# Performance work log

Hardware: AMD Instinct MI355X
Metric: run time of the kernel (lower is better)

## Reference

```python
import jax, jax.numpy as jnp
import numpy as np

B, C, H, W = 16, 512, 24, 24


def setup_inputs() -> dict:
    key = jax.random.key(0)
    ks = jax.random.split(key, 7)
    s = 0.02
    return {
        "x5": jax.random.normal(ks[0], (B, C, H, W), jnp.float32),
        "conv_w": jax.random.normal(ks[1], (C, C), jnp.float32) * s,
        "conv_b": jax.random.normal(ks[2], (C,), jnp.float32) * s,
        "q_w": jax.random.normal(ks[3], (C, C), jnp.float32) * s,
        "q_b": jax.random.normal(ks[4], (C,), jnp.float32) * s,
        "k_w": jax.random.normal(ks[5], (C, C), jnp.float32) * s,
        "k_b": jax.random.normal(ks[6], (C,), jnp.float32) * s,
    }


def _conv1x1(x, w, b):
    # 1x1 conv == channel matmul: (O,C) x (B,C,H,W) -> (B,O,H,W)
    return jnp.einsum('oc,bchw->bohw', w, x) + b[None, :, None, None]


def reference(x5, conv_w, conv_b, q_w, q_b, k_w, k_b):
    Bb, Cc, Hh, Ww = x5.shape
    scale = 1.0 / (Cc ** 0.5)
    x5 = _conv1x1(x5, conv_w, conv_b) + x5
    # my_SS2D source was not provided in the module; treated as identity (see notes)
    x00 = x5
    # cross-batch correlation: queries (B*H*W, C), keys (B, C, H*W)
    q = _conv1x1(x00, q_w, q_b).reshape(Bb, Cc, Hh * Ww).transpose(0, 2, 1).reshape(Bb * Hh * Ww, Cc)
    k = _conv1x1(x00, k_w, k_b).reshape(Bb, Cc, Hh * Ww)
    # scores: (B*H*W, B, H*W); max over locations, mean over images
    scores = jnp.einsum('nc,bcm->nbm', q, k) * scale
    x_w = scores.max(axis=-1).mean(axis=-1).reshape(Bb, Hh * Ww)
    x_w = jax.nn.softmax(x_w, axis=-1)
    # channel-wise L2 normalize (F.normalize, eps=1e-12)
    nrm = jnp.sqrt(jnp.sum(x5 * x5, axis=1, keepdims=True))
    norm0 = x5 / jnp.maximum(nrm, 1e-12)
    # top-1 (equality-based) seed mask per image
    x_w_max = x_w.max(axis=-1, keepdims=True)
    mask = (x_w == x_w_max).astype(x5.dtype).reshape(Bb, 1, Hh, Ww)
    seeds = (norm0 * mask).sum(axis=(2, 3))  # (B, C)
    # seeded 1x1-conv correlation (eval mode -> relu): (B, B_seeds, H, W)
    corr = jax.nn.relu(jnp.einsum('bchw,sc->bshw', norm0, seeds)).mean(axis=1).reshape(Bb, Hh * Ww)
    mn = corr.min(axis=-1, keepdims=True)
    mx = corr.max(axis=-1, keepdims=True)
    cormap = ((corr - mn) / (mx - mn + 1e-12)).reshape(Bb, 1, Hh, Ww)
    x51 = x5 * cormap
    proto1 = jnp.mean(x51, axis=(0, 2, 3), keepdims=True)  # (1, C, 1, 1)
    return (x5, proto1, x5 * proto1 + x51, mask)
```

## Files before the change

### kernel.cpp

```cpp
#include <hip/hip_runtime.h>
#include <math.h>

#define BB   16
#define CC   512
#define HWW  576
#define NN   9216
#define CHW  (CC*HWW)
#define TOT  (BB*CHW)
#define SCALE 0.044194173824159216f
#define FRAGB 9437184

typedef __attribute__((ext_vector_type(8))) __bf16 bf16x8;
typedef __attribute__((ext_vector_type(4))) float f32x4;

#define AS1 __attribute__((address_space(1)))
#define AS3 __attribute__((address_space(3)))

static __device__ __forceinline__ void gload_lds16(const void* g, void* l)
{
    __builtin_amdgcn_global_load_lds((AS1 const void*)g, (AS3 void*)l, 16, 0, 0);
}


__global__ __launch_bounds__(256)
void prep_x_kernel(const float* __restrict__ X, __bf16* __restrict__ Xhi,
                   __bf16* __restrict__ Xlo)
{
    int g = blockIdx.x * 256 + threadIdx.x;
    int n = g % NN;
    int co = g / NN;
    int c0 = co * 8;
    int bimg = n / HWW, mm = n % HWW;
    const float* src = X + (size_t)bimg * CHW + mm;
    union { __bf16 h[8]; float4 f4; } uh, ul;
#pragma unroll
    for (int j = 0; j < 8; j++) {
        float v = src[(size_t)(c0 + j) * HWW];
        __bf16 h = (__bf16)v;
        uh.h[j] = h;
        ul.h[j] = (__bf16)(v - (float)h);
    }
    int Cb = c0 >> 6, s = (c0 >> 5) & 1, q8 = (c0 >> 3) & 3;
    int T = n >> 6, g4 = (n >> 4) & 3, Lm = n & 15;
    size_t off = (size_t)(Cb * 144 + T) * 4096 + (s * 4 + g4) * 512 + (size_t)((q8 << 4) | Lm) * 8;
    *(float4*)&Xhi[off] = uh.f4;
    *(float4*)&Xlo[off] = ul.f4;
}

__global__ __launch_bounds__(256)
void prep_w_kernel(const float* __restrict__ cw, const float* __restrict__ qw,
                   const float* __restrict__ kw, __bf16* __restrict__ cwhi,
                   __bf16* __restrict__ cwlo, __bf16* __restrict__ qwf,
                   __bf16* __restrict__ kwf)
{
    int y = blockIdx.y;
    const float* W = (y == 0) ? cw : (y == 1) ? qw : kw;
    __bf16* dh = (y == 0) ? cwhi : (y == 1) ? qwf : kwf;
    int g = blockIdx.x * 256 + threadIdx.x;
    int o = g >> 6;
    int c0 = (g & 63) * 8;
    union { __bf16 h[8]; float4 f4; } uh, ul;
#pragma unroll
    for (int j = 0; j < 8; j++) {
        float v = W[(size_t)o * CC + c0 + j];
        __bf16 h = (__bf16)v;
        uh.h[j] = h;
        ul.h[j] = (__bf16)(v - (float)h);
    }
    int Cb = c0 >> 6, s = (c0 >> 5) & 1, q8 = (c0 >> 3) & 3;
    int To = o >> 6, g4 = (o >> 4) & 3, Lm = o & 15;
    size_t off = (size_t)(Cb * 8 + To) * 4096 + (s * 4 + g4) * 512 + (size_t)((q8 << 4) | Lm) * 8;
    *(float4*)&dh[off] = uh.f4;
    if (y == 0) *(float4*)&cwlo[off] = ul.f4;
}

__global__ __launch_bounds__(256)
void conv1_mfma_kernel(const float* __restrict__ X, const __bf16* __restrict__ Whi,
                       const __bf16* __restrict__ Wlo, const __bf16* __restrict__ Xhi,
                       const __bf16* __restrict__ Xlo, const float* __restrict__ bias,
                       float* __restrict__ Y, __bf16* __restrict__ Yfrag)
{
    __shared__ __bf16 lAh[8192], lAl[8192], lBh[8192], lBl[8192];
    int tid = threadIdx.x, lane = tid & 63, wv = tid >> 6;
    int wo = wv >> 1, wm = wv & 1;
    int m0 = blockIdx.x * 128;
    int o0 = blockIdx.y * 128;
    int oT0 = blockIdx.y * 2, mT0 = blockIdx.x * 2;

    f32x4 acc[4][4];
#pragma unroll
    for (int i = 0; i < 4; i++)
#pragma unroll
        for (int j = 0; j < 4; j++) acc[i][j] = (f32x4){0.f, 0.f, 0.f, 0.f};

    for (int Cb = 0; Cb < 8; Cb++) {
        const float4* gAh = (const float4*)(Whi + (size_t)(Cb * 8 + oT0) * 4096);
        const float4* gAl = (const float4*)(Wlo + (size_t)(Cb * 8 + oT0) * 4096);
        const float4* gBh = (const float4*)(Xhi + (size_t)(Cb * 144 + mT0) * 4096);
        const float4* gBl = (const float4*)(Xlo + (size_t)(Cb * 144 + mT0) * 4096);
#pragma unroll
        for (int i = 0; i < 4; i++) {
            int eb = wv * 256 + i * 64;
            gload_lds16(gAh + eb + lane, (float4*)lAh + eb);
            gload_lds16(gAl + eb + lane, (float4*)lAl + eb);
            gload_lds16(gBh + eb + lane, (float4*)lBh + eb);
            gload_lds16(gBl + eb + lane, (float4*)lBl + eb);
        }
        __syncthreads();
#pragma unroll
        for (int s = 0; s < 2; s++) {
            bf16x8 ah[4], al[4], bh[4], bl[4];
#pragma unroll
            for (int ga = 0; ga < 4; ga++) {
                ah[ga] = *(const bf16x8*)&lAh[wo * 4096 + (s * 4 + ga) * 512 + lane * 8];
                al[ga] = *(const bf16x8*)&lAl[wo * 4096 + (s * 4 + ga) * 512 + lane * 8];
            }
#pragma unroll
            for (int gb = 0; gb < 4; gb++) {
                bh[gb] = *(const bf16x8*)&lBh[wm * 4096 + (s * 4 + gb) * 512 + lane * 8];
                bl[gb] = *(const bf16x8*)&lBl[wm * 4096 + (s * 4 + gb) * 512 + lane * 8];
            }
#pragma unroll
            for (int ga = 0; ga < 4; ga++)
#pragma unroll
                for (int gb = 0; gb < 4; gb++) {
                    acc[ga][gb] = __builtin_amdgcn_mfma_f32_16x16x32_bf16(ah[ga], bh[gb], acc[ga][gb], 0, 0, 0);
                    acc[ga][gb] = __builtin_amdgcn_mfma_f32_16x16x32_bf16(ah[ga], bl[gb], acc[ga][gb], 0, 0, 0);
                    acc[ga][gb] = __builtin_amdgcn_mfma_f32_16x16x32_bf16(al[ga], bh[gb], acc[ga][gb], 0, 0, 0);
                }
        }
        __syncthreads();
    }

    int quad = lane >> 4, col = lane & 15;
#pragma unroll
    for (int ga = 0; ga < 4; ga++) {
        int ob = o0 + wo * 64 + ga * 16 + quad * 4;
        float bs[4];
#pragma unroll
        for (int r = 0; r < 4; r++) bs[r] = bias[ob + r];
        int Cb2 = ob >> 6, s2 = (ob >> 5) & 1, q8 = (ob >> 3) & 3, j0 = ob & 7;
#pragma unroll
        for (int gb = 0; gb < 4; gb++) {
            int n = m0 + wm * 64 + gb * 16 + col;
            int T = n >> 6, g4 = (n >> 4) & 3, Lm = n & 15;
            int bimg = n / HWW, mm = n % HWW;
            size_t xb = (size_t)bimg * CHW + mm;
            union { __bf16 h[4]; float2 f2; } u;
#pragma unroll
            for (int r = 0; r < 4; r++) {
                float v = acc[ga][gb][r] + bs[r] + X[xb + (size_t)(ob + r) * HWW];
                Y[xb + (size_t)(ob + r) * HWW] = v;
                u.h[r] = (__bf16)v;
            }
            *(float2*)&Yfrag[(size_t)(Cb2 * 144 + T) * 4096 + (s2 * 4 + g4) * 512 + (size_t)((q8 << 4) | Lm) * 8 + j0] = u.f2;
        }
    }
}

__global__ __launch_bounds__(256)
void convqk_mfma_kernel(const __bf16* __restrict__ qwf, const __bf16* __restrict__ kwf,
                        const float* __restrict__ qb, const float* __restrict__ kb,
                        const __bf16* __restrict__ Xf, __bf16* __restrict__ Oq,
                        __bf16* __restrict__ Ok)
{
    const __bf16* Wf = blockIdx.z ? kwf : qwf;
    const float* bias = blockIdx.z ? kb : qb;
    __bf16* Of = blockIdx.z ? Ok : Oq;

    __shared__ __bf16 lA[8192], lB[8192];
    int tid = threadIdx.x, lane = tid & 63, wv = tid >> 6;
    int wo = wv >> 1, wm = wv & 1;
    int m0 = blockIdx.x * 128;
    int o0 = blockIdx.y * 128;
    int oT0 = blockIdx.y * 2, mT0 = blockIdx.x * 2;

    f32x4 acc[4][4];
#pragma unroll
    for (int i = 0; i < 4; i++)
#pragma unroll
        for (int j = 0; j < 4; j++) acc[i][j] = (f32x4){0.f, 0.f, 0.f, 0.f};

    for (int Cb = 0; Cb < 8; Cb++) {
        const float4* gA = (const float4*)(Wf + (size_t)(Cb * 8 + oT0) * 4096);
        const float4* gB = (const float4*)(Xf + (size_t)(Cb * 144 + mT0) * 4096);
#pragma unroll
        for (int i = 0; i < 4; i++) {
            int eb = wv * 256 + i * 64;
            gload_lds16(gA + eb + lane, (float4*)lA + eb);
            gload_lds16(gB + eb + lane, (float4*)lB + eb);
        }
        __syncthreads();
#pragma unroll
        for (int s = 0; s < 2; s++) {
            bf16x8 af[4], bf[4];
#pragma unroll
            for (int ga = 0; ga < 4; ga++)
                af[ga] = *(const bf16x8*)&lA[wo * 4096 + (s * 4 + ga) * 512 + lane * 8];
#pragma unroll
            for (int gb = 0; gb < 4; gb++)
                bf[gb] = *(const bf16x8*)&lB[wm * 4096 + (s * 4 + gb) * 512 + lane * 8];
#pragma unroll
            for (int ga = 0; ga < 4; ga++)
#pragma unroll
                for (int gb = 0; gb < 4; gb++)
                    acc[ga][gb] = __builtin_amdgcn_mfma_f32_16x16x32_bf16(af[ga], bf[gb], acc[ga][gb], 0, 0, 0);
        }
        __syncthreads();
    }

    int quad = lane >> 4, col = lane & 15;
#pragma unroll
    for (int ga = 0; ga < 4; ga++) {
        int ob = o0 + wo * 64 + ga * 16 + quad * 4;
        float bs[4];
#pragma unroll
        for (int r = 0; r < 4; r++) bs[r] = bias[ob + r];
        int Cb2 = ob >> 6, s2 = (ob >> 5) & 1, q8 = (ob >> 3) & 3, j0 = ob & 7;
#pragma unroll
        for (int gb = 0; gb < 4; gb++) {
            int n = m0 + wm * 64 + gb * 16 + col;
            int T = n >> 6, g4 = (n >> 4) & 3, Lm = n & 15;
            union { __bf16 h[4]; float2 f2; } u;
#pragma unroll
            for (int r = 0; r < 4; r++) u.h[r] = (__bf16)(acc[ga][gb][r] + bs[r]);
            *(float2*)&Of[(size_t)(Cb2 * 144 + T) * 4096 + (s2 * 4 + g4) * 512 + (size_t)((q8 << 4) | Lm) * 8 + j0] = u.f2;
        }
    }
}

__global__ __launch_bounds__(256)
void scores_mfma_kernel(const __bf16* __restrict__ Qf, const __bf16* __restrict__ Kf,
                        float* __restrict__ maxv3, int bidoff)
{
    __shared__ __bf16 ldsQ[8192];
    __shared__ __bf16 ldsK[12288];

    int tid = threadIdx.x, lane = tid & 63, wv = tid >> 6;
    int wq = wv >> 1, wk = wv & 1;
    int bid = blockIdx.x + bidoff;
    int by = bid % 48;
    int bx = bid / 48;
    int n0 = bx * 128;
    int b = by / 3, mt = by % 3;

    f32x4 acc[4][6];
#pragma unroll
    for (int ga = 0; ga < 4; ga++)
#pragma unroll
        for (int t = 0; t < 6; t++) acc[ga][t] = (f32x4){0.f, 0.f, 0.f, 0.f};

    const float4* gq = (const float4*)(Qf + (size_t)(bx * 2) * 4096);
    const float4* gk = (const float4*)(Kf + (size_t)(b * 9 + mt * 3) * 4096);
    const int CSTRIDE = 144 * 4096 / 8;

    for (int C = 0; C < 8; C++) {
#pragma unroll
        for (int i = 0; i < 4; i++) {
            int eb = wv * 256 + i * 64;
            gload_lds16(gq + eb + lane, (float4*)ldsQ + eb);
        }
#pragma unroll
        for (int i = 0; i < 6; i++) {
            int eb = wv * 384 + i * 64;
            gload_lds16(gk + eb + lane, (float4*)ldsK + eb);
        }
        gq += CSTRIDE;
        gk += CSTRIDE;
        __syncthreads();
#pragma unroll
        for (int s = 0; s < 2; s++) {
            bf16x8 af[4];
#pragma unroll
            for (int ga = 0; ga < 4; ga++)
                af[ga] = *(const bf16x8*)&ldsQ[wq * 4096 + (s * 4 + ga) * 512 + lane * 8];
#pragma unroll
            for (int t = 0; t < 6; t++) {
                int mkl = wk * 96 + t * 16;
                bf16x8 bfr = *(const bf16x8*)&ldsK[(mkl >> 6) * 4096 + (s * 4 + ((mkl >> 4) & 3)) * 512 + lane * 8];
#pragma unroll
                for (int ga = 0; ga < 4; ga++)
                    acc[ga][t] = __builtin_amdgcn_mfma_f32_16x16x32_bf16(af[ga], bfr, acc[ga][t], 0, 0, 0);
            }
        }
        __syncthreads();
    }

    float mg[4][4];
#pragma unroll
    for (int ga = 0; ga < 4; ga++)
#pragma unroll
        for (int r = 0; r < 4; r++) {
            float v = acc[ga][0][r];
#pragma unroll
            for (int t = 1; t < 6; t++) v = fmaxf(v, acc[ga][t][r]);
            mg[ga][r] = v;
        }
#pragma unroll
    for (int off = 1; off < 16; off <<= 1)
#pragma unroll
        for (int ga = 0; ga < 4; ga++)
#pragma unroll
            for (int r = 0; r < 4; r++)
                mg[ga][r] = fmaxf(mg[ga][r], __shfl_xor(mg[ga][r], off, 64));

    float (*redbuf)[2] = (float (*)[2])ldsQ;
    if ((lane & 15) == 0) {
        int quad = lane >> 4;
#pragma unroll
        for (int ga = 0; ga < 4; ga++)
#pragma unroll
            for (int r = 0; r < 4; r++)
                redbuf[wq * 64 + ga * 16 + quad * 4 + r][wk] = mg[ga][r];
    }
    __syncthreads();
    if (tid < 128) {
        float rv = fmaxf(redbuf[tid][0], redbuf[tid][1]) * SCALE;
        maxv3[((size_t)(n0 + tid) * BB + b) * 3 + mt] = rv;
    }
}

__global__ __launch_bounds__(576)
void topk_kernel(const float* __restrict__ maxv3, int* __restrict__ cand)
{
    __shared__ float sv[576];
    __shared__ float rv_[64];
    __shared__ int ri_[64];
    int bi = blockIdx.x, m = threadIdx.x;
    int n = bi * HWW + m;
    float v = 0.f;
#pragma unroll
    for (int t = 0; t < BB; t++) {
        const float* p = maxv3 + ((size_t)n * BB + t) * 3;
        v += fmaxf(fmaxf(p[0], p[1]), p[2]);
    }
    sv[m] = v;
    __syncthreads();
    for (int r = 0; r < 4; r++) {
        if (m < 64) {
            float bv = sv[m]; int bidx = m;
            for (int j = m + 64; j < 576; j += 64)
                if (sv[j] > bv) { bv = sv[j]; bidx = j; }
            rv_[m] = bv; ri_[m] = bidx;
        }
        __syncthreads();
        if (m == 0) {
            float bv = rv_[0]; int bidx = ri_[0];
            for (int j = 1; j < 64; j++)
                if (rv_[j] > bv) { bv = rv_[j]; bidx = ri_[j]; }
            cand[bi * 4 + r] = bidx;
            sv[bidx] = -3.4e38f;
        }
        __syncthreads();
    }
}

__global__ __launch_bounds__(256)
void refine_q_kernel(const float* __restrict__ x5, const float* __restrict__ qw,
                     const float* __restrict__ qb, const int* __restrict__ cand,
                     float* __restrict__ q_all)
{
    int og = blockIdx.x, cd = blockIdx.y;
    int bi = cd >> 2;
    int mstar = cand[cd];
    int tid = threadIdx.x, w = tid >> 6, lane = tid & 63;
    __shared__ float xcol[512];
    __shared__ float qrows[64];
    xcol[tid]       = x5[(size_t)bi * CHW + tid * HWW + mstar];
    xcol[tid + 256] = x5[(size_t)bi * CHW + (tid + 256) * HWW + mstar];
    __syncthreads();
#pragma unroll
    for (int i = 0; i < 16; i++) {
        int r = og * 64 + w * 16 + i;
        float p = 0.f;
#pragma unroll
        for (int it = 0; it < 8; it++) {
            int c = lane + it * 64;
            p = fmaf(qw[(size_t)r * 512 + c], xcol[c], p);
        }
        for (int off = 32; off; off >>= 1) p += __shfl_down(p, off, 64);
        if (lane == 0) qrows[w * 16 + i] = p;
    }
    __syncthreads();
    if (tid < 64) q_all[(size_t)cd * 512 + og * 64 + tid] = qrows[tid] + qb[og * 64 + tid];
}

__global__ __launch_bounds__(256)
void refine_u2_kernel(const float* __restrict__ kw, const float* __restrict__ kb,
                      const float* __restrict__ q_all, float* __restrict__ u_all,
                      float* __restrict__ qkbg)
{
    int tg = blockIdx.x, cd = blockIdx.y;
    int tid = threadIdx.x;
    __shared__ float qs[512];
    qs[tid]       = q_all[(size_t)cd * 512 + tid];
    qs[tid + 256] = q_all[(size_t)cd * 512 + tid + 256];
    __syncthreads();
    int t = tg * 256 + tid;
    float u = 0.f;
    for (int o = 0; o < 512; o++)
        u = fmaf(kw[(size_t)o * 512 + t], qs[o], u);
    u_all[(size_t)cd * 512 + t] = u;
    if (tg == 0) {
        float pk = qs[tid] * kb[tid] + qs[tid + 256] * kb[tid + 256];
        for (int off = 32; off; off >>= 1) pk += __shfl_down(pk, off, 64);
        __shared__ float pr[4];
        if ((tid & 63) == 0) pr[tid >> 6] = pk;
        __syncthreads();
        if (tid == 0) qkbg[cd] = pr[0] + pr[1] + pr[2] + pr[3];
    }
}

__global__ __launch_bounds__(256)
void refine_max_kernel(const float* __restrict__ x5, const float* __restrict__ u_all,
                       float* __restrict__ maxex9)
{
    int bp = blockIdx.x, cg = blockIdx.y, mc = blockIdx.z;
    int tid = threadIdx.x, mi = tid & 63, cs = tid >> 6;
    int m0 = mc * 64;
    __shared__ float us[16 * 512];
    __shared__ float red[256];
    for (int e = tid; e < 16 * 512; e += 256) us[e] = u_all[(size_t)cg * 16 * 512 + e];
    __syncthreads();

    float acc[16];
#pragma unroll
    for (int j = 0; j < 16; j++) acc[j] = 0.f;
    const float* xb = x5 + (size_t)bp * CHW + m0 + mi;
    for (int cc = 0; cc < 128; cc++) {
        int c = cs * 128 + cc;
        float x = xb[(size_t)c * HWW];
#pragma unroll
        for (int j = 0; j < 16; j++)
            acc[j] = fmaf(us[j * 512 + c], x, acc[j]);
    }

#pragma unroll
    for (int j = 0; j < 16; j++) {
        red[tid] = acc[j];
        __syncthreads();
        if (tid < 64) {
            float v = red[tid] + red[tid + 64] + red[tid + 128] + red[tid + 192];
            for (int off = 32; off; off >>= 1) v = fmaxf(v, __shfl_xor(v, off, 64));
            if (tid == 0) maxex9[((size_t)(cg * 16 + j) * BB + bp) * 9 + mc] = v;
        }
        __syncthreads();
    }
}

__global__ __launch_bounds__(576)
void mask_kernel(const float* __restrict__ maxex9, const float* __restrict__ qkbg,
                 const int* __restrict__ cand, float* __restrict__ maskout)
{
    int bi = blockIdx.x, m = threadIdx.x;
    __shared__ float ve[4];
    __shared__ int chosen;
    if (m < 4) {
        int cd = bi * 4 + m;
        float sacc = 0.f;
#pragma unroll
        for (int t = 0; t < BB; t++) {
            const float* p = maxex9 + ((size_t)cd * BB + t) * 9;
            float mv = p[0];
#pragma unroll
            for (int z = 1; z < 9; z++) mv = fmaxf(mv, p[z]);
            sacc += mv;
        }
        ve[m] = sacc * (1.f / 16.f) + qkbg[cd];
    }
    __syncthreads();
    if (m == 0) {
        int best = 0; float bv = ve[0];
        for (int j = 1; j < 4; j++) if (ve[j] > bv) { bv = ve[j]; best = j; }
        chosen = cand[bi * 4 + best];
    }
    __syncthreads();
    maskout[bi * HWW + m] = (m == chosen) ? 1.f : 0.f;
}

__global__ __launch_bounds__(256)
void norm_kernel(const float* __restrict__ X5, float* __restrict__ invb)
{
    int b = blockIdx.y;
    int m0 = blockIdx.x * 64;
    int mi = threadIdx.x & 63, cs = threadIdx.x >> 6;
    float s = 0.f;
    for (int c = cs; c < CC; c += 4) {
        float x = X5[b * CHW + c * HWW + m0 + mi];
        s = fmaf(x, x, s);
    }
    __shared__ float red[4][64];
    red[cs][mi] = s;
    __syncthreads();
    if (cs == 0) {
        float t = red[0][mi] + red[1][mi] + red[2][mi] + red[3][mi];
        invb[b * HWW + m0 + mi] = 1.0f / fmaxf(sqrtf(t), 1e-12f);
    }
}

__global__ __launch_bounds__(256)
void seeds_kernel(const float* __restrict__ X5, const float* __restrict__ invb,
                  const float* __restrict__ maskf, float* __restrict__ seeds)
{
    int s = blockIdx.y;
    int c = blockIdx.x * 4 + (threadIdx.x >> 6);
    int mi = threadIdx.x & 63;
    float acc = 0.f;
    for (int mt = 0; mt < 9; mt++) {
        int m = mt * 64 + mi;
        float w = invb[s * HWW + m] * maskf[s * HWW + m];
        acc = fmaf(X5[s * CHW + c * HWW + m], w, acc);
    }
    for (int off = 32; off > 0; off >>= 1) acc += __shfl_down(acc, off, 64);
    if (mi == 0) seeds[s * CC + c] = acc;
}

__global__ __launch_bounds__(256)
void corr_kernel(const float* __restrict__ X5, const float* __restrict__ invb,
                 const float* __restrict__ seeds, float* __restrict__ corr)
{
    __shared__ float sd[16 * 512];
    __shared__ float xs[64][65];
    __shared__ float red[4][64];
    int b = blockIdx.y;
    int m0 = blockIdx.x * 64;
    int tid = threadIdx.x;
    int mi = tid & 63, sg = tid >> 6;

    for (int e = tid; e < 16 * 512; e += 256) sd[e] = seeds[e];

    float acc[4] = {0.f, 0.f, 0.f, 0.f};
    for (int c0 = 0; c0 < CC; c0 += 64) {
        __syncthreads();
        for (int e = tid; e < 4096; e += 256) {
            int mm = e & 63, kk = e >> 6;
            xs[kk][mm] = X5[b * CHW + (c0 + kk) * HWW + m0 + mm];
        }
        __syncthreads();
#pragma unroll
        for (int kk = 0; kk < 64; kk++) {
            float xv = xs[kk][mi];
#pragma unroll
            for (int t = 0; t < 4; t++)
                acc[t] = fmaf(xv, sd[(sg * 4 + t) * CC + c0 + kk], acc[t]);
        }
    }
    float r = 0.f;
#pragma unroll
    for (int t = 0; t < 4; t++) r += fmaxf(acc[t], 0.f);
    red[sg][mi] = r;
    __syncthreads();
    if (sg == 0) {
        float tot = red[0][mi] + red[1][mi] + red[2][mi] + red[3][mi];
        corr[b * HWW + m0 + mi] = invb[b * HWW + m0 + mi] * tot * (1.0f / 16.0f);
    }
}

__global__ __launch_bounds__(576)
void cormap_kernel(const float* __restrict__ corr, float* __restrict__ cormap)
{
    __shared__ float sv[576];
    __shared__ float smn[64], smx[64];
    __shared__ float s_mn, s_mx;
    int b = blockIdx.x;
    int m = threadIdx.x;
    float v = corr[b * HWW + m];
    sv[m] = v;
    __syncthreads();
    if (m < 64) {
        float mn = sv[m], mx = sv[m];
        for (int j = m + 64; j < 576; j += 64) { mn = fminf(mn, sv[j]); mx = fmaxf(mx, sv[j]); }
        smn[m] = mn; smx[m] = mx;
    }
    __syncthreads();
    if (m == 0) {
        float mn = smn[0], mx = smx[0];
        for (int j = 1; j < 64; j++) { mn = fminf(mn, smn[j]); mx = fmaxf(mx, smx[j]); }
        s_mn = mn; s_mx = mx;
    }
    __syncthreads();
    cormap[b * HWW + m] = (v - s_mn) / (s_mx - s_mn + 1e-12f);
}

__global__ __launch_bounds__(256)
void proto_kernel(const float* __restrict__ X5, const float* __restrict__ cormap,
                  float* __restrict__ proto1)
{
    int c = blockIdx.x;
    int tid = threadIdx.x;
    float acc = 0.f;
    for (int p = tid; p < NN; p += 256) {
        int b = p / HWW, m = p % HWW;
        acc = fmaf(X5[b * CHW + c * HWW + m], cormap[p], acc);
    }
    for (int off = 32; off > 0; off >>= 1) acc += __shfl_down(acc, off, 64);
    __shared__ float red[4];
    if ((tid & 63) == 0) red[tid >> 6] = acc;
    __syncthreads();
    if (tid == 0) proto1[c] = (red[0] + red[1] + red[2] + red[3]) * (1.0f / (float)NN);
}

__global__ __launch_bounds__(256)
void final_kernel(const float* __restrict__ X5, const float* __restrict__ proto1,
                  const float* __restrict__ cormap, float* __restrict__ out3)
{
    int idx = blockIdx.x * 256 + threadIdx.x;
    if (idx >= TOT) return;
    int b = idx / CHW;
    int r = idx % CHW;
    int c = r / HWW;
    int m = r % HWW;
    float x = X5[idx];
    out3[idx] = x * (proto1[c] + cormap[b * HWW + m]);
}

extern "C" void kernel_launch(void* const* d_in, const int* in_sizes, int n_in,
                              void* d_out, int out_size, void* d_ws, size_t ws_size,
                              hipStream_t stream)
{
    const float* x  = (const float*)d_in[0];
    const float* cw = (const float*)d_in[1];
    const float* cb = (const float*)d_in[2];
    const float* qw = (const float*)d_in[3];
    const float* qb = (const float*)d_in[4];
    const float* kw = (const float*)d_in[5];
    const float* kb = (const float*)d_in[6];

    float* out     = (float*)d_out;
    float* x5o     = out;
    float* proto1  = out + TOT;
    float* out3    = out + TOT + 512;
    float* maskout = out + TOT + 512 + TOT;

    char* o3 = (char*)out3;
    __bf16* xlo    = (__bf16*)o3;
    __bf16* qfrag  = (__bf16*)o3;
    __bf16* x5frag = (__bf16*)(o3 + FRAGB);

    char* ws = (char*)d_ws;
    __bf16* xhi   = (__bf16*)ws;
    __bf16* kfrag = (__bf16*)ws;
    __bf16* cwhi  = (__bf16*)(ws + FRAGB);
    __bf16* cwlo  = (__bf16*)(ws + FRAGB + 524288);
    __bf16* qwf   = (__bf16*)(ws + FRAGB + 2 * 524288);
    __bf16* kwf   = (__bf16*)(ws + FRAGB + 3 * 524288);
    char* p = ws + FRAGB + 4 * 524288;
    float* maxv3  = (float*)p;   p += (size_t)NN * BB * 3 * 4;
    int*   cand   = (int*)p;     p += 256;
    float* q_all  = (float*)p;   p += 64 * 512 * 4;
    float* u_all  = (float*)p;   p += 64 * 512 * 4;
    float* qkbg   = (float*)p;   p += 256;
    float* maxex9 = (float*)p;   p += 64 * BB * 9 * 4;
    float* invb   = (float*)p;   p += NN * 4;
    float* corr   = (float*)p;   p += NN * 4;
    float* cmap   = (float*)p;   p += NN * 4;
    float* seeds  = (float*)p;   p += BB * CC * 4;

    prep_x_kernel<<<NN * 64 / 256, 256, 0, stream>>>(x, xhi, xlo);
    prep_w_kernel<<<dim3(128, 3), 256, 0, stream>>>(cw, qw, kw, cwhi, cwlo, qwf, kwf);

    conv1_mfma_kernel<<<dim3(NN / 128, 4), 256, 0, stream>>>(x, cwhi, cwlo, xhi, xlo, cb, x5o, x5frag);
    convqk_mfma_kernel<<<dim3(NN / 128, 4, 2), 256, 0, stream>>>(qwf, kwf, qb, kb, x5frag, qfrag, kfrag);

    scores_mfma_kernel<<<1728, 256, 0, stream>>>(qfrag, kfrag, maxv3, 0);
    scores_mfma_kernel<<<1728, 256, 0, stream>>>(qfrag, kfrag, maxv3, 1728);

    topk_kernel<<<BB, HWW, 0, stream>>>(maxv3, cand);
    refine_q_kernel<<<dim3(8, 64), 256, 0, stream>>>(x5o, qw, qb, cand, q_all);
    refine_u2_kernel<<<dim3(2, 64), 256, 0, stream>>>(kw, kb, q_all, u_all, qkbg);
    refine_max_kernel<<<dim3(BB, 4, 9), 256, 0, stream>>>(x5o, u_all, maxex9);
    mask_kernel<<<BB, HWW, 0, stream>>>(maxex9, qkbg, cand, maskout);

    norm_kernel<<<dim3(9, BB), 256, 0, stream>>>(x5o, invb);
    seeds_kernel<<<dim3(CC / 4, BB), 256, 0, stream>>>(x5o, invb, maskout, seeds);
    corr_kernel<<<dim3(9, BB), 256, 0, stream>>>(x5o, invb, seeds, corr);
    cormap_kernel<<<BB, HWW, 0, stream>>>(corr, cmap);
    proto_kernel<<<CC, 256, 0, stream>>>(x5o, cmap, proto1);
    final_kernel<<<(TOT + 255) / 256, 256, 0, stream>>>(x5o, proto1, cmap, out3);
}
```

Baseline: 387.9 us.

## Load conv weights directly, merge refine kernels, direct seed gather, restructure reductions

The two conv MFMA kernels now read weight fragments straight from global memory into registers instead of staging them through LDS, which cuts LDS use and copy traffic. The two scores launches become one, and the q and u refine kernels are fused into a single per-candidate kernel. Seeds are gathered directly at the chosen index instead of a masked reduction over all positions. The refine_max reduction now uses a single barrier, proto drops its per-element div/mod, and final_kernel uses a 2D grid without index division. Direct global weight loads inside the MFMA loop could add latency if caching does not hide it.

```diff
diff --git a/kernel.cpp b/kernel.cpp
--- a/kernel.cpp
+++ b/kernel.cpp
@@ -80,7 +80,7 @@
                        const __bf16* __restrict__ Xlo, const float* __restrict__ bias,
                        float* __restrict__ Y, __bf16* __restrict__ Yfrag)
 {
-    __shared__ __bf16 lAh[8192], lAl[8192], lBh[8192], lBl[8192];
+    __shared__ __bf16 lBh[8192], lBl[8192];
     int tid = threadIdx.x, lane = tid & 63, wv = tid >> 6;
     int wo = wv >> 1, wm = wv & 1;
     int m0 = blockIdx.x * 128;
@@ -94,26 +94,24 @@
         for (int j = 0; j < 4; j++) acc[i][j] = (f32x4){0.f, 0.f, 0.f, 0.f};
 
     for (int Cb = 0; Cb < 8; Cb++) {
-        const float4* gAh = (const float4*)(Whi + (size_t)(Cb * 8 + oT0) * 4096);
-        const float4* gAl = (const float4*)(Wlo + (size_t)(Cb * 8 + oT0) * 4096);
         const float4* gBh = (const float4*)(Xhi + (size_t)(Cb * 144 + mT0) * 4096);
         const float4* gBl = (const float4*)(Xlo + (size_t)(Cb * 144 + mT0) * 4096);
 #pragma unroll
         for (int i = 0; i < 4; i++) {
             int eb = wv * 256 + i * 64;
-            gload_lds16(gAh + eb + lane, (float4*)lAh + eb);
-            gload_lds16(gAl + eb + lane, (float4*)lAl + eb);
             gload_lds16(gBh + eb + lane, (float4*)lBh + eb);
             gload_lds16(gBl + eb + lane, (float4*)lBl + eb);
         }
+        const __bf16* Ah = Whi + (size_t)(Cb * 8 + oT0 + wo) * 4096 + lane * 8;
+        const __bf16* Al = Wlo + (size_t)(Cb * 8 + oT0 + wo) * 4096 + lane * 8;
         __syncthreads();
 #pragma unroll
         for (int s = 0; s < 2; s++) {
             bf16x8 ah[4], al[4], bh[4], bl[4];
 #pragma unroll
             for (int ga = 0; ga < 4; ga++) {
-                ah[ga] = *(const bf16x8*)&lAh[wo * 4096 + (s * 4 + ga) * 512 + lane * 8];
-                al[ga] = *(const bf16x8*)&lAl[wo * 4096 + (s * 4 + ga) * 512 + lane * 8];
+                ah[ga] = *(const bf16x8*)&Ah[(s * 4 + ga) * 512];
+                al[ga] = *(const bf16x8*)&Al[(s * 4 + ga) * 512];
             }
 #pragma unroll
             for (int gb = 0; gb < 4; gb++) {
@@ -168,7 +166,7 @@
     const float* bias = blockIdx.z ? kb : qb;
     __bf16* Of = blockIdx.z ? Ok : Oq;
 
-    __shared__ __bf16 lA[8192], lB[8192];
+    __shared__ __bf16 lB[8192];
     int tid = threadIdx.x, lane = tid & 63, wv = tid >> 6;
     int wo = wv >> 1, wm = wv & 1;
     int m0 = blockIdx.x * 128;
@@ -182,21 +180,20 @@
         for (int j = 0; j < 4; j++) acc[i][j] = (f32x4){0.f, 0.f, 0.f, 0.f};
 
     for (int Cb = 0; Cb < 8; Cb++) {
-        const float4* gA = (const float4*)(Wf + (size_t)(Cb * 8 + oT0) * 4096);
         const float4* gB = (const float4*)(Xf + (size_t)(Cb * 144 + mT0) * 4096);
 #pragma unroll
         for (int i = 0; i < 4; i++) {
             int eb = wv * 256 + i * 64;
-            gload_lds16(gA + eb + lane, (float4*)lA + eb);
             gload_lds16(gB + eb + lane, (float4*)lB + eb);
         }
+        const __bf16* Aw = Wf + (size_t)(Cb * 8 + oT0 + wo) * 4096 + lane * 8;
         __syncthreads();
 #pragma unroll
         for (int s = 0; s < 2; s++) {
             bf16x8 af[4], bf[4];
 #pragma unroll
             for (int ga = 0; ga < 4; ga++)
-                af[ga] = *(const bf16x8*)&lA[wo * 4096 + (s * 4 + ga) * 512 + lane * 8];
+                af[ga] = *(const bf16x8*)&Aw[(s * 4 + ga) * 512];
 #pragma unroll
             for (int gb = 0; gb < 4; gb++)
                 bf[gb] = *(const bf16x8*)&lB[wm * 4096 + (s * 4 + gb) * 512 + lane * 8];
@@ -231,14 +228,14 @@
 
 __global__ __launch_bounds__(256)
 void scores_mfma_kernel(const __bf16* __restrict__ Qf, const __bf16* __restrict__ Kf,
-                        float* __restrict__ maxv3, int bidoff)
+                        float* __restrict__ maxv3)
 {
     __shared__ __bf16 ldsQ[8192];
     __shared__ __bf16 ldsK[12288];
 
     int tid = threadIdx.x, lane = tid & 63, wv = tid >> 6;
     int wq = wv >> 1, wk = wv & 1;
-    int bid = blockIdx.x + bidoff;
+    int bid = blockIdx.x;
     int by = bid % 48;
     int bx = bid / 48;
     int n0 = bx * 128;
@@ -356,22 +353,21 @@
 }
 
 __global__ __launch_bounds__(256)
-void refine_q_kernel(const float* __restrict__ x5, const float* __restrict__ qw,
-                     const float* __restrict__ qb, const int* __restrict__ cand,
-                     float* __restrict__ q_all)
-{
-    int og = blockIdx.x, cd = blockIdx.y;
+void refine_qu_kernel(const float* __restrict__ x5, const float* __restrict__ qw,
+                      const float* __restrict__ qb, const float* __restrict__ kw,
+                      const float* __restrict__ kb, const int* __restrict__ cand,
+                      float* __restrict__ u_all, float* __restrict__ qkbg)
+{
+    int cd = blockIdx.x;
     int bi = cd >> 2;
     int mstar = cand[cd];
     int tid = threadIdx.x, w = tid >> 6, lane = tid & 63;
-    __shared__ float xcol[512];
-    __shared__ float qrows[64];
+    __shared__ float xcol[512], qv[512];
     xcol[tid]       = x5[(size_t)bi * CHW + tid * HWW + mstar];
     xcol[tid + 256] = x5[(size_t)bi * CHW + (tid + 256) * HWW + mstar];
     __syncthreads();
-#pragma unroll
-    for (int i = 0; i < 16; i++) {
-        int r = og * 64 + w * 16 + i;
+    for (int i = 0; i < 128; i++) {
+        int r = w * 128 + i;
         float p = 0.f;
 #pragma unroll
         for (int it = 0; it < 8; it++) {
@@ -379,36 +375,23 @@
             p = fmaf(qw[(size_t)r * 512 + c], xcol[c], p);
         }
         for (int off = 32; off; off >>= 1) p += __shfl_down(p, off, 64);
-        if (lane == 0) qrows[w * 16 + i] = p;
-    }
-    __syncthreads();
-    if (tid < 64) q_all[(size_t)cd * 512 + og * 64 + tid] = qrows[tid] + qb[og * 64 + tid];
-}
-
-__global__ __launch_bounds__(256)
-void refine_u2_kernel(const float* __restrict__ kw, const float* __restrict__ kb,
-                      const float* __restrict__ q_all, float* __restrict__ u_all,
-                      float* __restrict__ qkbg)
-{
-    int tg = blockIdx.x, cd = blockIdx.y;
-    int tid = threadIdx.x;
-    __shared__ float qs[512];
-    qs[tid]       = q_all[(size_t)cd * 512 + tid];
-    qs[tid + 256] = q_all[(size_t)cd * 512 + tid + 256];
-    __syncthreads();
-    int t = tg * 256 + tid;
-    float u = 0.f;
-    for (int o = 0; o < 512; o++)
-        u = fmaf(kw[(size_t)o * 512 + t], qs[o], u);
-    u_all[(size_t)cd * 512 + t] = u;
-    if (tg == 0) {
-        float pk = qs[tid] * kb[tid] + qs[tid + 256] * kb[tid + 256];
-        for (int off = 32; off; off >>= 1) pk += __shfl_down(pk, off, 64);
-        __shared__ float pr[4];
-        if ((tid & 63) == 0) pr[tid >> 6] = pk;
-        __syncthreads();
-        if (tid == 0) qkbg[cd] = pr[0] + pr[1] + pr[2] + pr[3];
-    }
+        if (lane == 0) qv[r] = p + qb[r];
+    }
+    __syncthreads();
+    float u0 = 0.f, u1 = 0.f;
+    for (int o = 0; o < 512; o++) {
+        float qc = qv[o];
+        u0 = fmaf(kw[(size_t)o * 512 + tid], qc, u0);
+        u1 = fmaf(kw[(size_t)o * 512 + tid + 256], qc, u1);
+    }
+    u_all[(size_t)cd * 512 + tid] = u0;
+    u_all[(size_t)cd * 512 + tid + 256] = u1;
+    float pk = qv[tid] * kb[tid] + qv[tid + 256] * kb[tid + 256];
+    for (int off = 32; off; off >>= 1) pk += __shfl_down(pk, off, 64);
+    __shared__ float pr[4];
+    if (lane == 0) pr[w] = pk;
+    __syncthreads();
+    if (tid == 0) qkbg[cd] = pr[0] + pr[1] + pr[2] + pr[3];
 }
 
 __global__ __launch_bounds__(256)
@@ -419,7 +402,7 @@
     int tid = threadIdx.x, mi = tid & 63, cs = tid >> 6;
     int m0 = mc * 64;
     __shared__ float us[16 * 512];
-    __shared__ float red[256];
+    __shared__ float red[16][4][64];
     for (int e = tid; e < 16 * 512; e += 256) us[e] = u_all[(size_t)cg * 16 * 512 + e];
     __syncthreads();
 
@@ -434,23 +417,23 @@
         for (int j = 0; j < 16; j++)
             acc[j] = fmaf(us[j * 512 + c], x, acc[j]);
     }
-
-#pragma unroll
-    for (int j = 0; j < 16; j++) {
-        red[tid] = acc[j];
-        __syncthreads();
-        if (tid < 64) {
-            float v = red[tid] + red[tid + 64] + red[tid + 128] + red[tid + 192];
+#pragma unroll
+    for (int j = 0; j < 16; j++) red[j][cs][mi] = acc[j];
+    __syncthreads();
+    if (tid < 64) {
+#pragma unroll
+        for (int j = 0; j < 16; j++) {
+            float v = red[j][0][tid] + red[j][1][tid] + red[j][2][tid] + red[j][3][tid];
             for (int off = 32; off; off >>= 1) v = fmaxf(v, __shfl_xor(v, off, 64));
-            if (tid == 0) maxex9[((size_t)(cg * 16 + j) * BB + bp) * 9 + mc] = v;
-        }
-        __syncthreads();
+            if (tid == j) maxex9[((size_t)(cg * 16 + j) * BB + bp) * 9 + mc] = v;
+        }
     }
 }
 
 __global__ __launch_bounds__(576)
 void mask_kernel(const float* __restrict__ maxex9, const float* __restrict__ qkbg,
-                 const int* __restrict__ cand, float* __restrict__ maskout)
+                 const int* __restrict__ cand, float* __restrict__ maskout,
+                 int* __restrict__ chosenidx)
 {
     int bi = blockIdx.x, m = threadIdx.x;
     __shared__ float ve[4];
@@ -473,6 +456,7 @@
         int best = 0; float bv = ve[0];
         for (int j = 1; j < 4; j++) if (ve[j] > bv) { bv = ve[j]; best = j; }
         chosen = cand[bi * 4 + best];
+        chosenidx[bi] = chosen;
     }
     __syncthreads();
     maskout[bi * HWW + m] = (m == chosen) ? 1.f : 0.f;
@@ -498,21 +482,14 @@
     }
 }
 
-__global__ __launch_bounds__(256)
-void seeds_kernel(const float* __restrict__ X5, const float* __restrict__ invb,
-                  const float* __restrict__ maskf, float* __restrict__ seeds)
-{
-    int s = blockIdx.y;
-    int c = blockIdx.x * 4 + (threadIdx.x >> 6);
-    int mi = threadIdx.x & 63;
-    float acc = 0.f;
-    for (int mt = 0; mt < 9; mt++) {
-        int m = mt * 64 + mi;
-        float w = invb[s * HWW + m] * maskf[s * HWW + m];
-        acc = fmaf(X5[s * CHW + c * HWW + m], w, acc);
-    }
-    for (int off = 32; off > 0; off >>= 1) acc += __shfl_down(acc, off, 64);
-    if (mi == 0) seeds[s * CC + c] = acc;
+__global__ __launch_bounds__(512)
+void seeds_direct_kernel(const float* __restrict__ X5, const float* __restrict__ invb,
+                         const int* __restrict__ chosenidx, float* __restrict__ seeds)
+{
+    int s = blockIdx.x, c = threadIdx.x;
+    int mstar = chosenidx[s];
+    float w = invb[s * HWW + mstar];
+    seeds[s * CC + c] = X5[(size_t)s * CHW + (size_t)c * HWW + mstar] * w;
 }
 
 __global__ __launch_bounds__(256)
@@ -589,9 +566,11 @@
     int c = blockIdx.x;
     int tid = threadIdx.x;
     float acc = 0.f;
-    for (int p = tid; p < NN; p += 256) {
-        int b = p / HWW, m = p % HWW;
-        acc = fmaf(X5[b * CHW + c * HWW + m], cormap[p], acc);
+    for (int b = 0; b < BB; b++) {
+        const float* xp = X5 + (size_t)b * CHW + (size_t)c * HWW;
+        const float* cp = cormap + b * HWW;
+        for (int m = tid; m < HWW; m += 256)
+            acc = fmaf(xp[m], cp[m], acc);
     }
     for (int off = 32; off > 0; off >>= 1) acc += __shfl_down(acc, off, 64);
     __shared__ float red[4];
@@ -600,18 +579,19 @@
     if (tid == 0) proto1[c] = (red[0] + red[1] + red[2] + red[3]) * (1.0f / (float)NN);
 }
 
-__global__ __launch_bounds__(256)
+__global__ __launch_bounds__(192)
 void final_kernel(const float* __restrict__ X5, const float* __restrict__ proto1,
                   const float* __restrict__ cormap, float* __restrict__ out3)
 {
-    int idx = blockIdx.x * 256 + threadIdx.x;
-    if (idx >= TOT) return;
-    int b = idx / CHW;
-    int r = idx % CHW;
-    int c = r / HWW;
-    int m = r % HWW;
-    float x = X5[idx];
-    out3[idx] = x * (proto1[c] + cormap[b * HWW + m]);
+    int c = blockIdx.x, b = blockIdx.y;
+    size_t base = (size_t)b * CHW + (size_t)c * HWW;
+    float pc = proto1[c];
+    const float* cp = cormap + b * HWW;
+#pragma unroll
+    for (int k = 0; k < 3; k++) {
+        int m = threadIdx.x + k * 192;
+        out3[base + m] = X5[base + m] * (pc + cp[m]);
+    }
 }
 
 extern "C" void kernel_launch(void* const* d_in, const int* in_sizes, int n_in,
@@ -647,7 +627,7 @@
     char* p = ws + FRAGB + 4 * 524288;
     float* maxv3  = (float*)p;   p += (size_t)NN * BB * 3 * 4;
     int*   cand   = (int*)p;     p += 256;
-    float* q_all  = (float*)p;   p += 64 * 512 * 4;
+    int*   chosenidx = (int*)p;  p += 256;
     float* u_all  = (float*)p;   p += 64 * 512 * 4;
     float* qkbg   = (float*)p;   p += 256;
     float* maxex9 = (float*)p;   p += 64 * BB * 9 * 4;
@@ -662,19 +642,17 @@
     conv1_mfma_kernel<<<dim3(NN / 128, 4), 256, 0, stream>>>(x, cwhi, cwlo, xhi, xlo, cb, x5o, x5frag);
     convqk_mfma_kernel<<<dim3(NN / 128, 4, 2), 256, 0, stream>>>(qwf, kwf, qb, kb, x5frag, qfrag, kfrag);
 
-    scores_mfma_kernel<<<1728, 256, 0, stream>>>(qfrag, kfrag, maxv3, 0);
-    scores_mfma_kernel<<<1728, 256, 0, stream>>>(qfrag, kfrag, maxv3, 1728);
+    scores_mfma_kernel<<<3456, 256, 0, stream>>>(qfrag, kfrag, maxv3);
 
     topk_kernel<<<BB, HWW, 0, stream>>>(maxv3, cand);
-    refine_q_kernel<<<dim3(8, 64), 256, 0, stream>>>(x5o, qw, qb, cand, q_all);
-    refine_u2_kernel<<<dim3(2, 64), 256, 0, stream>>>(kw, kb, q_all, u_all, qkbg);
+    refine_qu_kernel<<<64, 256, 0, stream>>>(x5o, qw, qb, kw, kb, cand, u_all, qkbg);
     refine_max_kernel<<<dim3(BB, 4, 9), 256, 0, stream>>>(x5o, u_all, maxex9);
-    mask_kernel<<<BB, HWW, 0, stream>>>(maxex9, qkbg, cand, maskout);
+    mask_kernel<<<BB, HWW, 0, stream>>>(maxex9, qkbg, cand, maskout, chosenidx);
 
     norm_kernel<<<dim3(9, BB), 256, 0, stream>>>(x5o, invb);
-    seeds_kernel<<<dim3(CC / 4, BB), 256, 0, stream>>>(x5o, invb, maskout, seeds);
+    seeds_direct_kernel<<<BB, 512, 0, stream>>>(x5o, invb, chosenidx, seeds);
     corr_kernel<<<dim3(9, BB), 256, 0, stream>>>(x5o, invb, seeds, corr);
     cormap_kernel<<<BB, HWW, 0, stream>>>(corr, cmap);
     proto_kernel<<<CC, 256, 0, stream>>>(x5o, cmap, proto1);
-    final_kernel<<<(TOT + 255) / 256, 256, 0, stream>>>(x5o, proto1, cmap, out3);
-}
+    final_kernel<<<dim3(CC, BB), 192, 0, stream>>>(x5o, proto1, cmap, out3);
+}
```

Measured after the change: 444.4 us. 14.6% more time.
